# Performance work log

Measured on AMD Instinct MI355X. Metric: run time of the kernel, lower is better.

The kernel has to match this reference:

```python
import jax, jax.numpy as jnp
import numpy as np

CODEBOOK_SIZE = 1024
EMB_DIM = 64


def setup_inputs() -> dict:
    key = jax.random.key(0)
    k1, k2 = jax.random.split(key)
    z = jax.random.normal(k1, (4, EMB_DIM, 32, 32, 32), dtype=jnp.float32)
    embedding = jax.random.normal(k2, (CODEBOOK_SIZE, EMB_DIM), dtype=jnp.float32)
    return {"z": z, "embedding": embedding}


def reference(z, embedding):
    # z: [b, c, h, w, d], embedding: [K, c]
    b, c, h, w, d = z.shape
    K = embedding.shape[0]
    # flatten to [N, c] with channels last (matches permute(0,2,3,4,1).reshape)
    zf = jnp.transpose(z, (0, 2, 3, 4, 1)).reshape(-1, c)
    # squared L2 distance to each codebook entry: ||z||^2 - 2 z.e + ||e||^2
    dist = (
        jnp.sum(zf * zf, axis=1, keepdims=True)
        - 2.0 * zf @ embedding.T
        + jnp.sum(embedding * embedding, axis=1)[None, :]
    )  # [N, K]
    min_encoding_indices = jnp.argmin(dist, axis=1)  # [N]
    # one-hot @ embedding == gather (same math, no NxK materialization)
    z_q = embedding[min_encoding_indices]  # [N, c]
    z_q = jnp.transpose(z_q.reshape(b, h, w, d, c), (0, 4, 1, 2, 3))
    # straight-through estimator
    z_q = z + jax.lax.stop_gradient(z_q - z)
    # perplexity from mean one-hot occupancy
    n_tokens = zf.shape[0]
    e_mean = jnp.bincount(min_encoding_indices, length=K).astype(zf.dtype) / n_tokens
    perplexity = jnp.exp(-jnp.sum(e_mean * jnp.log(e_mean + 1e-10)))
    loss = jnp.asarray(0.0, dtype=z.dtype)
    return (
        z_q,
        loss,
        perplexity,
        min_encoding_indices.reshape(b, h, w, d),
        jnp.mean(dist),
    )
```

## Files before the change

kernel.cpp:

```cpp
#include <hip/hip_runtime.h>

#define CH     64
#define KC     1024
#define SP     32768
#define NBATCH 4
#define NTOK   (NBATCH * SP)
#define MTOK   64
#define SZZ    68
#define ECH    256
#define SZEB   72
#define CAP    16
#define MARGIN 3.0f

#define OFF_ZQ   0
#define OFF_LOSS (NBATCH * CH * SP)
#define OFF_PERP (OFF_LOSS + 1)
#define OFF_IDX  (OFF_PERP + 1)
#define OFF_MEAN (OFF_IDX + NTOK)


typedef __attribute__((ext_vector_type(8))) short  s16x8;
typedef __attribute__((ext_vector_type(4))) float  f32x4;

__device__ __forceinline__ unsigned short f2bf(float f) {
    unsigned int u = __float_as_uint(f);
    return (unsigned short)((u + 0x7fffu + ((u >> 16) & 1u)) >> 16);
}

__device__ __forceinline__ float exact_dist(const float* zrow,
                                            const float* __restrict__ emb,
                                            const float* enl, int c) {
    const float4* er = (const float4*)(emb + (size_t)c * CH);
    float a0 = 0.f, a1 = 0.f, a2 = 0.f, a3 = 0.f;
#pragma unroll
    for (int j = 0; j < 16; ++j) {
        float4 e4 = er[j];
        a0 = fmaf(zrow[4 * j + 0], e4.x, a0);
        a1 = fmaf(zrow[4 * j + 1], e4.y, a1);
        a2 = fmaf(zrow[4 * j + 2], e4.z, a2);
        a3 = fmaf(zrow[4 * j + 3], e4.w, a3);
    }
    return enl[c] - 2.f * ((a0 + a1) + (a2 + a3));
}

__global__ __launch_bounds__(256) void prep(const float* __restrict__ e,
                                            int* __restrict__ hist,
                                            float* __restrict__ sums,
                                            float* __restrict__ sum_zc,
                                            float* __restrict__ sum_ec,
                                            float* __restrict__ enorm,
                                            unsigned short* __restrict__ eb) {
    const int tid = threadIdx.x;
    const int bk = blockIdx.x;
    if (bk < 4) {
        int k = bk * 256 + tid;
        const float4* row = (const float4*)(e + (size_t)k * CH);
        float n = 0.f;
#pragma unroll
        for (int j = 0; j < CH / 4; ++j) {
            float4 v = row[j];
            n += v.x * v.x + v.y * v.y + v.z * v.z + v.w * v.w;
        }
        enorm[k] = n;
    } else if (bk == 4) {
        if (tid == 0) sums[0] = 0.f;
        if (tid < 64) sum_zc[tid] = 0.f;
        __shared__ float ls1[256];
        __shared__ float r2[4];
        int c = tid & 63;
        int strip = tid >> 6;
        float s1 = 0.f, s2 = 0.f;
        for (int k = strip * 256; k < strip * 256 + 256; ++k) {
            float v = e[k * CH + c];
            s1 += v;
            s2 = fmaf(v, v, s2);
        }
        ls1[tid] = s1;
        for (int off = 32; off; off >>= 1) s2 += __shfl_down(s2, off);
        if ((tid & 63) == 0) r2[tid >> 6] = s2;
        __syncthreads();
        if (strip == 0) sum_ec[c] = ls1[c] + ls1[64 + c] + ls1[128 + c] + ls1[192 + c];
        if (tid == 0) sums[1] = r2[0] + r2[1] + r2[2] + r2[3];
    } else if (bk < 9) {
        hist[(bk - 5) * 256 + tid] = 0;
    } else {
        int base = (bk - 9) * 16384;
        for (int j = 0; j < 64; ++j) {
            int i = base + tid + j * 256;
            eb[i] = f2bf(e[i]);
        }
    }
}

__global__ __launch_bounds__(256, 2) void vq_main(const float* __restrict__ z,
                                                  const float* __restrict__ emb,
                                                  const unsigned short* __restrict__ eb,
                                                  const float* __restrict__ enorm,
                                                  float* __restrict__ out,
                                                  int* __restrict__ hist,
                                                  float* __restrict__ sums,
                                                  float* __restrict__ sum_zc) {
    __shared__ float zl[MTOK * SZZ];
    __shared__ unsigned short ebl[ECH * SZEB];
    __shared__ float enorm_l[KC];
    __shared__ float dmin_l[MTOK];
    __shared__ float zs1[256], zs2[256];
    __shared__ int   cand[MTOK][CAP];
    __shared__ int   ccnt[MTOK];
    __shared__ int   fi[MTOK];

    const int tid = threadIdx.x;
    const int w = tid >> 6;
    const int lane = tid & 63;
    const int n15 = lane & 15;
    const int q = lane >> 4;
    const int t0 = blockIdx.x * MTOK;
    const int bb = t0 >> 15;
    const int s0 = t0 & (SP - 1);

    {
        const float* zbase = z + ((size_t)bb * CH) * SP + s0;
#pragma unroll
        for (int j = 0; j < 4; ++j) {
            int idx = tid + j * 256;
            int c = idx >> 4;
            int tq = idx & 15;
            float4 v = *(const float4*)(zbase + (size_t)c * SP + tq * 4);
            zl[(4 * tq + 0) * SZZ + c] = v.x;
            zl[(4 * tq + 1) * SZZ + c] = v.y;
            zl[(4 * tq + 2) * SZZ + c] = v.z;
            zl[(4 * tq + 3) * SZZ + c] = v.w;
        }
#pragma unroll
        for (int j = 0; j < 4; ++j) enorm_l[tid + j * 256] = enorm[tid + j * 256];
        if (tid < MTOK) ccnt[tid] = 0;
    }
    __syncthreads();

    s16x8 A0, A1;
    {
        const float* zrow = &zl[(w * 16 + n15) * SZZ];
        float4 za = *(const float4*)(zrow + q * 8);
        float4 zb = *(const float4*)(zrow + q * 8 + 4);
        float4 zc = *(const float4*)(zrow + 32 + q * 8);
        float4 zd = *(const float4*)(zrow + 32 + q * 8 + 4);
        A0[0] = (short)f2bf(za.x); A0[1] = (short)f2bf(za.y);
        A0[2] = (short)f2bf(za.z); A0[3] = (short)f2bf(za.w);
        A0[4] = (short)f2bf(zb.x); A0[5] = (short)f2bf(zb.y);
        A0[6] = (short)f2bf(zb.z); A0[7] = (short)f2bf(zb.w);
        A1[0] = (short)f2bf(zc.x); A1[1] = (short)f2bf(zc.y);
        A1[2] = (short)f2bf(zc.z); A1[3] = (short)f2bf(zc.w);
        A1[4] = (short)f2bf(zd.x); A1[5] = (short)f2bf(zd.y);
        A1[6] = (short)f2bf(zd.z); A1[7] = (short)f2bf(zd.w);
    }
    const unsigned short* ebq = ebl + (size_t)n15 * SZEB + q * 8;

    float bmin[4] = {3.4e38f, 3.4e38f, 3.4e38f, 3.4e38f};
    for (int ch = 0; ch < 4; ++ch) {
        __syncthreads();
#pragma unroll
        for (int rep = 0; rep < 8; ++rep) {
            int i = tid + rep * 256;
            int row = i >> 3, j = i & 7;
            ((float4*)&ebl[row * SZEB])[j] =
                ((const float4*)(eb + (size_t)(ch * ECH + row) * CH))[j];
        }
        __syncthreads();
        for (int ct = 0; ct < 16; ++ct) {
            const unsigned short* p = ebq + ct * 16 * SZEB;
            s16x8 B0 = *(const s16x8*)p;
            s16x8 B1 = *(const s16x8*)(p + 32);
            f32x4 acc = {0.f, 0.f, 0.f, 0.f};
            acc = __builtin_amdgcn_mfma_f32_16x16x32_bf16(A0, B0, acc, 0, 0, 0);
            acc = __builtin_amdgcn_mfma_f32_16x16x32_bf16(A1, B1, acc, 0, 0, 0);
            float en = enorm_l[ch * ECH + ct * 16 + n15];
#pragma unroll
            for (int r = 0; r < 4; ++r) {
                float d = fmaf(-2.f, acc[r], en);
                bmin[r] = fminf(bmin[r], d);
            }
        }
    }
#pragma unroll
    for (int off = 1; off < 16; off <<= 1)
#pragma unroll
        for (int r = 0; r < 4; ++r)
            bmin[r] = fminf(bmin[r], __shfl_xor(bmin[r], off));
    if (n15 == 0)
#pragma unroll
        for (int r = 0; r < 4; ++r) dmin_l[w * 16 + 4 * q + r] = bmin[r];
    __syncthreads();

    float thr[4];
#pragma unroll
    for (int r = 0; r < 4; ++r) thr[r] = dmin_l[w * 16 + 4 * q + r] + MARGIN;
    for (int cc = 0; cc < 4; ++cc) {
        int ch = (cc == 0) ? 3 : (cc - 1);
        if (cc) {
            __syncthreads();
#pragma unroll
            for (int rep = 0; rep < 8; ++rep) {
                int i = tid + rep * 256;
                int row = i >> 3, j = i & 7;
                ((float4*)&ebl[row * SZEB])[j] =
                    ((const float4*)(eb + (size_t)(ch * ECH + row) * CH))[j];
            }
            __syncthreads();
        }
        for (int ct = 0; ct < 16; ++ct) {
            const unsigned short* p = ebq + ct * 16 * SZEB;
            s16x8 B0 = *(const s16x8*)p;
            s16x8 B1 = *(const s16x8*)(p + 32);
            f32x4 acc = {0.f, 0.f, 0.f, 0.f};
            acc = __builtin_amdgcn_mfma_f32_16x16x32_bf16(A0, B0, acc, 0, 0, 0);
            acc = __builtin_amdgcn_mfma_f32_16x16x32_bf16(A1, B1, acc, 0, 0, 0);
            float en = enorm_l[ch * ECH + ct * 16 + n15];
#pragma unroll
            for (int r = 0; r < 4; ++r) {
                float d = fmaf(-2.f, acc[r], en);
                if (d <= thr[r]) {
                    int t = w * 16 + 4 * q + r;
                    int pos = atomicAdd(&ccnt[t], 1);
                    if (pos < CAP) cand[t][pos] = ch * ECH + ct * 16 + n15;
                }
            }
        }
    }
    __syncthreads();

    if (tid < MTOK) {
        int t = tid;
        const float* zrow = &zl[t * SZZ];
        int cnt = ccnt[t];
        float best = 3.4e38f;
        int bi = 0;
        if (cnt <= CAP) {
            for (int j = 0; j < cnt; ++j) {
                int c = cand[t][j];
                float d = exact_dist(zrow, emb, enorm_l, c);
                if (d < best || (d == best && c < bi)) { best = d; bi = c; }
            }
        } else {
            for (int c = 0; c < KC; ++c) {
                float d = exact_dist(zrow, emb, enorm_l, c);
                if (d < best) { best = d; bi = c; }
            }
        }
        fi[t] = bi;
        out[OFF_IDX + t0 + t] = (float)bi;
        atomicAdd(&hist[bi], 1);
    }
    __syncthreads();

#pragma unroll
    for (int j = 0; j < 16; ++j) {
        int idx = tid + j * 256;
        int c = idx >> 6;
        int t = idx & 63;
        int code = fi[t];
        float ev = emb[(size_t)code * CH + c];
        float zv = zl[t * SZZ + c];
        out[OFF_ZQ + ((size_t)bb * CH + c) * SP + s0 + t] = zv + (ev - zv);
    }

    {
        int c = tid >> 2, qq = tid & 3;
        float s1 = 0.f, s2 = 0.f;
        for (int tt = 0; tt < 16; ++tt) {
            float v = zl[(qq * 16 + tt) * SZZ + c];
            s1 += v;
            s2 = fmaf(v, v, s2);
        }
        zs1[tid] = s1;
        zs2[tid] = s2;
    }
    __syncthreads();
    if (tid < 64) {
        float a = zs1[4 * tid] + zs1[4 * tid + 1] + zs1[4 * tid + 2] + zs1[4 * tid + 3];
        atomicAdd(&sum_zc[tid], a);
        float bsum = zs2[4 * tid] + zs2[4 * tid + 1] + zs2[4 * tid + 2] + zs2[4 * tid + 3];
        for (int off = 32; off; off >>= 1) bsum += __shfl_down(bsum, off);
        if (tid == 0) atomicAdd(&sums[0], bsum);
    }
}

__global__ __launch_bounds__(1024) void finalize(const int* __restrict__ hist,
                                                 const float* __restrict__ sums,
                                                 const float* __restrict__ sum_zc,
                                                 const float* __restrict__ sum_ec,
                                                 float* __restrict__ out) {
    __shared__ float red[1024];
    int k = threadIdx.x;
    float p = (float)hist[k] * (1.0f / (float)NTOK);
    red[k] = p * logf(p + 1e-10f);
    __syncthreads();
    for (int off = 512; off; off >>= 1) {
        if (k < off) red[k] += red[k + off];
        __syncthreads();
    }
    if (k == 0) {
        out[OFF_PERP] = expf(-red[0]);
        out[OFF_LOSS] = 0.f;
        double dot = 0.0;
        for (int c = 0; c < CH; ++c) dot += (double)sum_zc[c] * (double)sum_ec[c];
        double mean = ((double)KC * (double)sums[0] + (double)NTOK * (double)sums[1] - 2.0 * dot)
                      / ((double)NTOK * (double)KC);
        out[OFF_MEAN] = (float)mean;
    }
}

extern "C" void kernel_launch(void* const* d_in, const int* in_sizes, int n_in,
                              void* d_out, int out_size, void* d_ws, size_t ws_size,
                              hipStream_t stream) {
    const float* z   = (const float*)d_in[0];
    const float* emb = (const float*)d_in[1];
    float* out = (float*)d_out;

    int*            hist   = (int*)d_ws;
    float*          sums   = (float*)d_ws + 1024;
    float*          sum_zc = (float*)d_ws + 1026;
    float*          sum_ec = (float*)d_ws + 1090;
    float*          enorm  = (float*)d_ws + 1154;
    unsigned short* eb     = (unsigned short*)((int*)d_ws + 4096);

    prep<<<13, 256, 0, stream>>>(emb, hist, sums, sum_zc, sum_ec, enorm, eb);
    vq_main<<<NTOK / MTOK, 256, 0, stream>>>(z, emb, eb, enorm, out, hist, sums, sum_zc);
    finalize<<<1, 1024, 0, stream>>>(hist, sums, sum_zc, sum_ec, out);
}
```

Before: 227.3 us.

## Double tokens per block and stream bf16 codebook from global memory without LDS staging

Each wave now handles 32 tokens instead of 16, so every codebook fragment feeds two MFMA pairs. The bf16 codebook and its norms are read straight from global/L2 rather than staged through shared memory, which removes the chunk loads and barriers from both MFMA passes. Dropping those LDS buffers lets occupancy rise to 4 blocks per CU. In exchange the kernel depends on the cache for codebook reuse, candidate capacity halves to 8 (so more tokens may hit the full 1024-code exact fallback), and the z-statistics scratch now reuses the candidate buffer.

```diff
diff --git a/kernel.cpp b/kernel.cpp
--- a/kernel.cpp
+++ b/kernel.cpp
@@ -5,11 +5,9 @@
 #define SP     32768
 #define NBATCH 4
 #define NTOK   (NBATCH * SP)
-#define MTOK   64
+#define MTOK   128
 #define SZZ    68
-#define ECH    256
-#define SZEB   72
-#define CAP    16
+#define CAP    8
 #define MARGIN 3.0f
 
 #define OFF_ZQ   0
@@ -29,7 +27,7 @@
 
 __device__ __forceinline__ float exact_dist(const float* zrow,
                                             const float* __restrict__ emb,
-                                            const float* enl, int c) {
+                                            const float* __restrict__ enl, int c) {
     const float4* er = (const float4*)(emb + (size_t)c * CH);
     float a0 = 0.f, a1 = 0.f, a2 = 0.f, a3 = 0.f;
 #pragma unroll
@@ -92,7 +90,17 @@
     }
 }
 
-__global__ __launch_bounds__(256, 2) void vq_main(const float* __restrict__ z,
+#define MK8(A, ptr)                                            \
+    {                                                          \
+        float4 _a = *(const float4*)(ptr);                     \
+        float4 _b = *(const float4*)((ptr) + 4);               \
+        A[0] = (short)f2bf(_a.x); A[1] = (short)f2bf(_a.y);    \
+        A[2] = (short)f2bf(_a.z); A[3] = (short)f2bf(_a.w);    \
+        A[4] = (short)f2bf(_b.x); A[5] = (short)f2bf(_b.y);    \
+        A[6] = (short)f2bf(_b.z); A[7] = (short)f2bf(_b.w);    \
+    }
+
+__global__ __launch_bounds__(256, 4) void vq_main(const float* __restrict__ z,
                                                   const float* __restrict__ emb,
                                                   const unsigned short* __restrict__ eb,
                                                   const float* __restrict__ enorm,
@@ -101,10 +109,6 @@
                                                   float* __restrict__ sums,
                                                   float* __restrict__ sum_zc) {
     __shared__ float zl[MTOK * SZZ];
-    __shared__ unsigned short ebl[ECH * SZEB];
-    __shared__ float enorm_l[KC];
-    __shared__ float dmin_l[MTOK];
-    __shared__ float zs1[256], zs2[256];
     __shared__ int   cand[MTOK][CAP];
     __shared__ int   ccnt[MTOK];
     __shared__ int   fi[MTOK];
@@ -121,108 +125,93 @@
     {
         const float* zbase = z + ((size_t)bb * CH) * SP + s0;
 #pragma unroll
-        for (int j = 0; j < 4; ++j) {
-            int idx = tid + j * 256;
-            int c = idx >> 4;
-            int tq = idx & 15;
+        for (int rep = 0; rep < 8; ++rep) {
+            int idx = tid + rep * 256;
+            int c = idx >> 5;
+            int tq = idx & 31;
             float4 v = *(const float4*)(zbase + (size_t)c * SP + tq * 4);
             zl[(4 * tq + 0) * SZZ + c] = v.x;
             zl[(4 * tq + 1) * SZZ + c] = v.y;
             zl[(4 * tq + 2) * SZZ + c] = v.z;
             zl[(4 * tq + 3) * SZZ + c] = v.w;
         }
-#pragma unroll
-        for (int j = 0; j < 4; ++j) enorm_l[tid + j * 256] = enorm[tid + j * 256];
         if (tid < MTOK) ccnt[tid] = 0;
     }
     __syncthreads();
 
-    s16x8 A0, A1;
+    s16x8 A0, A1, A2, A3;
     {
-        const float* zrow = &zl[(w * 16 + n15) * SZZ];
-        float4 za = *(const float4*)(zrow + q * 8);
-        float4 zb = *(const float4*)(zrow + q * 8 + 4);
-        float4 zc = *(const float4*)(zrow + 32 + q * 8);
-        float4 zd = *(const float4*)(zrow + 32 + q * 8 + 4);
-        A0[0] = (short)f2bf(za.x); A0[1] = (short)f2bf(za.y);
-        A0[2] = (short)f2bf(za.z); A0[3] = (short)f2bf(za.w);
-        A0[4] = (short)f2bf(zb.x); A0[5] = (short)f2bf(zb.y);
-        A0[6] = (short)f2bf(zb.z); A0[7] = (short)f2bf(zb.w);
-        A1[0] = (short)f2bf(zc.x); A1[1] = (short)f2bf(zc.y);
-        A1[2] = (short)f2bf(zc.z); A1[3] = (short)f2bf(zc.w);
-        A1[4] = (short)f2bf(zd.x); A1[5] = (short)f2bf(zd.y);
-        A1[6] = (short)f2bf(zd.z); A1[7] = (short)f2bf(zd.w);
-    }
-    const unsigned short* ebq = ebl + (size_t)n15 * SZEB + q * 8;
-
-    float bmin[4] = {3.4e38f, 3.4e38f, 3.4e38f, 3.4e38f};
-    for (int ch = 0; ch < 4; ++ch) {
-        __syncthreads();
-#pragma unroll
-        for (int rep = 0; rep < 8; ++rep) {
-            int i = tid + rep * 256;
-            int row = i >> 3, j = i & 7;
-            ((float4*)&ebl[row * SZEB])[j] =
-                ((const float4*)(eb + (size_t)(ch * ECH + row) * CH))[j];
-        }
-        __syncthreads();
-        for (int ct = 0; ct < 16; ++ct) {
-            const unsigned short* p = ebq + ct * 16 * SZEB;
-            s16x8 B0 = *(const s16x8*)p;
-            s16x8 B1 = *(const s16x8*)(p + 32);
-            f32x4 acc = {0.f, 0.f, 0.f, 0.f};
-            acc = __builtin_amdgcn_mfma_f32_16x16x32_bf16(A0, B0, acc, 0, 0, 0);
-            acc = __builtin_amdgcn_mfma_f32_16x16x32_bf16(A1, B1, acc, 0, 0, 0);
-            float en = enorm_l[ch * ECH + ct * 16 + n15];
-#pragma unroll
-            for (int r = 0; r < 4; ++r) {
-                float d = fmaf(-2.f, acc[r], en);
-                bmin[r] = fminf(bmin[r], d);
+        const float* zr0 = &zl[(w * 32 + n15) * SZZ];
+        const float* zr1 = zr0 + 16 * SZZ;
+        MK8(A0, zr0 + q * 8)
+        MK8(A1, zr0 + 32 + q * 8)
+        MK8(A2, zr1 + q * 8)
+        MK8(A3, zr1 + 32 + q * 8)
+    }
+
+    const unsigned short* ebp = eb + (size_t)n15 * CH + q * 8;
+    const float* enp = enorm + n15;
+
+    float bmin0[4] = {3.4e38f, 3.4e38f, 3.4e38f, 3.4e38f};
+    float bmin1[4] = {3.4e38f, 3.4e38f, 3.4e38f, 3.4e38f};
+#pragma unroll 4
+    for (int ct = 0; ct < 64; ++ct) {
+        const unsigned short* pr = ebp + (size_t)ct * (16 * CH);
+        s16x8 B0 = *(const s16x8*)pr;
+        s16x8 B1 = *(const s16x8*)(pr + 32);
+        float en = enp[ct * 16];
+        f32x4 acc0 = {0.f, 0.f, 0.f, 0.f};
+        f32x4 acc1 = {0.f, 0.f, 0.f, 0.f};
+        acc0 = __builtin_amdgcn_mfma_f32_16x16x32_bf16(A0, B0, acc0, 0, 0, 0);
+        acc0 = __builtin_amdgcn_mfma_f32_16x16x32_bf16(A1, B1, acc0, 0, 0, 0);
+        acc1 = __builtin_amdgcn_mfma_f32_16x16x32_bf16(A2, B0, acc1, 0, 0, 0);
+        acc1 = __builtin_amdgcn_mfma_f32_16x16x32_bf16(A3, B1, acc1, 0, 0, 0);
+#pragma unroll
+        for (int r = 0; r < 4; ++r) {
+            bmin0[r] = fminf(bmin0[r], fmaf(-2.f, acc0[r], en));
+            bmin1[r] = fminf(bmin1[r], fmaf(-2.f, acc1[r], en));
+        }
+    }
+#pragma unroll
+    for (int off = 1; off < 16; off <<= 1)
+#pragma unroll
+        for (int r = 0; r < 4; ++r) {
+            bmin0[r] = fminf(bmin0[r], __shfl_xor(bmin0[r], off));
+            bmin1[r] = fminf(bmin1[r], __shfl_xor(bmin1[r], off));
+        }
+    float thr0[4], thr1[4];
+#pragma unroll
+    for (int r = 0; r < 4; ++r) {
+        thr0[r] = bmin0[r] + MARGIN;
+        thr1[r] = bmin1[r] + MARGIN;
+    }
+
+    const int tb0 = w * 32 + 4 * q;
+    const int tb1 = tb0 + 16;
+#pragma unroll 4
+    for (int ct = 0; ct < 64; ++ct) {
+        const unsigned short* pr = ebp + (size_t)ct * (16 * CH);
+        s16x8 B0 = *(const s16x8*)pr;
+        s16x8 B1 = *(const s16x8*)(pr + 32);
+        float en = enp[ct * 16];
+        f32x4 acc0 = {0.f, 0.f, 0.f, 0.f};
+        f32x4 acc1 = {0.f, 0.f, 0.f, 0.f};
+        acc0 = __builtin_amdgcn_mfma_f32_16x16x32_bf16(A0, B0, acc0, 0, 0, 0);
+        acc0 = __builtin_amdgcn_mfma_f32_16x16x32_bf16(A1, B1, acc0, 0, 0, 0);
+        acc1 = __builtin_amdgcn_mfma_f32_16x16x32_bf16(A2, B0, acc1, 0, 0, 0);
+        acc1 = __builtin_amdgcn_mfma_f32_16x16x32_bf16(A3, B1, acc1, 0, 0, 0);
+        int code = ct * 16 + n15;
+#pragma unroll
+        for (int r = 0; r < 4; ++r) {
+            float d0 = fmaf(-2.f, acc0[r], en);
+            if (d0 <= thr0[r]) {
+                int pos = atomicAdd(&ccnt[tb0 + r], 1);
+                if (pos < CAP) cand[tb0 + r][pos] = code;
             }
-        }
-    }
-#pragma unroll
-    for (int off = 1; off < 16; off <<= 1)
-#pragma unroll
-        for (int r = 0; r < 4; ++r)
-            bmin[r] = fminf(bmin[r], __shfl_xor(bmin[r], off));
-    if (n15 == 0)
-#pragma unroll
-        for (int r = 0; r < 4; ++r) dmin_l[w * 16 + 4 * q + r] = bmin[r];
-    __syncthreads();
-
-    float thr[4];
-#pragma unroll
-    for (int r = 0; r < 4; ++r) thr[r] = dmin_l[w * 16 + 4 * q + r] + MARGIN;
-    for (int cc = 0; cc < 4; ++cc) {
-        int ch = (cc == 0) ? 3 : (cc - 1);
-        if (cc) {
-            __syncthreads();
-#pragma unroll
-            for (int rep = 0; rep < 8; ++rep) {
-                int i = tid + rep * 256;
-                int row = i >> 3, j = i & 7;
-                ((float4*)&ebl[row * SZEB])[j] =
-                    ((const float4*)(eb + (size_t)(ch * ECH + row) * CH))[j];
-            }
-            __syncthreads();
-        }
-        for (int ct = 0; ct < 16; ++ct) {
-            const unsigned short* p = ebq + ct * 16 * SZEB;
-            s16x8 B0 = *(const s16x8*)p;
-            s16x8 B1 = *(const s16x8*)(p + 32);
-            f32x4 acc = {0.f, 0.f, 0.f, 0.f};
-            acc = __builtin_amdgcn_mfma_f32_16x16x32_bf16(A0, B0, acc, 0, 0, 0);
-            acc = __builtin_amdgcn_mfma_f32_16x16x32_bf16(A1, B1, acc, 0, 0, 0);
-            float en = enorm_l[ch * ECH + ct * 16 + n15];
-#pragma unroll
-            for (int r = 0; r < 4; ++r) {
-                float d = fmaf(-2.f, acc[r], en);
-                if (d <= thr[r]) {
-                    int t = w * 16 + 4 * q + r;
-                    int pos = atomicAdd(&ccnt[t], 1);
-                    if (pos < CAP) cand[t][pos] = ch * ECH + ct * 16 + n15;
-                }
+            float d1 = fmaf(-2.f, acc1[r], en);
+            if (d1 <= thr1[r]) {
+                int pos = atomicAdd(&ccnt[tb1 + r], 1);
+                if (pos < CAP) cand[tb1 + r][pos] = code;
             }
         }
     }
@@ -237,12 +226,12 @@
         if (cnt <= CAP) {
             for (int j = 0; j < cnt; ++j) {
                 int c = cand[t][j];
-                float d = exact_dist(zrow, emb, enorm_l, c);
+                float d = exact_dist(zrow, emb, enorm, c);
                 if (d < best || (d == best && c < bi)) { best = d; bi = c; }
             }
         } else {
             for (int c = 0; c < KC; ++c) {
-                float d = exact_dist(zrow, emb, enorm_l, c);
+                float d = exact_dist(zrow, emb, enorm, c);
                 if (d < best) { best = d; bi = c; }
             }
         }
@@ -253,34 +242,39 @@
     __syncthreads();
 
 #pragma unroll
-    for (int j = 0; j < 16; ++j) {
-        int idx = tid + j * 256;
-        int c = idx >> 6;
-        int t = idx & 63;
+    for (int rep = 0; rep < 32; ++rep) {
+        int idx = tid + rep * 256;
+        int c = idx >> 7;
+        int t = idx & 127;
         int code = fi[t];
         float ev = emb[(size_t)code * CH + c];
         float zv = zl[t * SZZ + c];
         out[OFF_ZQ + ((size_t)bb * CH + c) * SP + s0 + t] = zv + (ev - zv);
     }
 
-    {
-        int c = tid >> 2, qq = tid & 3;
+    float* zs = reinterpret_cast<float*>(cand);
+#pragma unroll
+    for (int h = 0; h < 2; ++h) {
+        const int c = tid >> 2, qq = tid & 3;
         float s1 = 0.f, s2 = 0.f;
+#pragma unroll
         for (int tt = 0; tt < 16; ++tt) {
-            float v = zl[(qq * 16 + tt) * SZZ + c];
+            float v = zl[(h * 64 + qq * 16 + tt) * SZZ + c];
             s1 += v;
             s2 = fmaf(v, v, s2);
         }
-        zs1[tid] = s1;
-        zs2[tid] = s2;
-    }
-    __syncthreads();
-    if (tid < 64) {
-        float a = zs1[4 * tid] + zs1[4 * tid + 1] + zs1[4 * tid + 2] + zs1[4 * tid + 3];
-        atomicAdd(&sum_zc[tid], a);
-        float bsum = zs2[4 * tid] + zs2[4 * tid + 1] + zs2[4 * tid + 2] + zs2[4 * tid + 3];
-        for (int off = 32; off; off >>= 1) bsum += __shfl_down(bsum, off);
-        if (tid == 0) atomicAdd(&sums[0], bsum);
+        zs[tid] = s1;
+        zs[256 + tid] = s2;
+        __syncthreads();
+        if (tid < 64) {
+            float a = zs[4 * tid] + zs[4 * tid + 1] + zs[4 * tid + 2] + zs[4 * tid + 3];
+            atomicAdd(&sum_zc[tid], a);
+            float bsum = zs[256 + 4 * tid] + zs[256 + 4 * tid + 1]
+                       + zs[256 + 4 * tid + 2] + zs[256 + 4 * tid + 3];
+            for (int off = 32; off; off >>= 1) bsum += __shfl_down(bsum, off);
+            if (tid == 0) atomicAdd(&sums[0], bsum);
+        }
+        __syncthreads();
     }
 }
 
```

After: 609.1 us. 168% more time.

## Prefetch codebook chunks through registers with swizzled LDS and higher occupancy

Applied to the files above, without the earlier changes.

Halves the codebook chunk staged in LDS to 128 entries. While the MFMA work runs on the current chunk, the next chunk is loaded into registers and then written to LDS, so global loads overlap compute in both the min pass and the candidate pass. Row padding is replaced by an XOR swizzle to avoid bank conflicts. CAP is cut to 8 and the reduction scratch reuses the candidate buffer, so the smaller LDS footprint lets launch bounds ask for 4 blocks per CU. The trade-offs are more barriers per chunk, added register pressure from the prefetch, and a greater chance of falling back to the full exact scan when a token has more than 8 near candidates.

```diff
diff --git a/kernel.cpp b/kernel.cpp
--- a/kernel.cpp
+++ b/kernel.cpp
@@ -7,9 +7,8 @@
 #define NTOK   (NBATCH * SP)
 #define MTOK   64
 #define SZZ    68
-#define ECH    256
-#define SZEB   72
-#define CAP    16
+#define ECH    128
+#define CAP    8
 #define MARGIN 3.0f
 
 #define OFF_ZQ   0
@@ -92,7 +91,7 @@
     }
 }
 
-__global__ __launch_bounds__(256, 2) void vq_main(const float* __restrict__ z,
+__global__ __launch_bounds__(256, 4) void vq_main(const float* __restrict__ z,
                                                   const float* __restrict__ emb,
                                                   const unsigned short* __restrict__ eb,
                                                   const float* __restrict__ enorm,
@@ -101,10 +100,9 @@
                                                   float* __restrict__ sums,
                                                   float* __restrict__ sum_zc) {
     __shared__ float zl[MTOK * SZZ];
-    __shared__ unsigned short ebl[ECH * SZEB];
+    __shared__ __align__(16) unsigned short ebl[ECH * 64];
     __shared__ float enorm_l[KC];
     __shared__ float dmin_l[MTOK];
-    __shared__ float zs1[256], zs2[256];
     __shared__ int   cand[MTOK][CAP];
     __shared__ int   ccnt[MTOK];
     __shared__ int   fi[MTOK];
@@ -117,6 +115,25 @@
     const int t0 = blockIdx.x * MTOK;
     const int bb = t0 >> 15;
     const int s0 = t0 & (SP - 1);
+
+    const int sg  = tid & 7;
+    const int sr0 = tid >> 3;
+    const int sgd = sg ^ (sr0 & 7);
+    float4 g0, g1, g2, g3;
+#define STAGE_LOAD(cb)                                                      \
+    {                                                                       \
+        g0 = ((const float4*)(eb + (size_t)((cb) + sr0) * CH))[sg];         \
+        g1 = ((const float4*)(eb + (size_t)((cb) + sr0 + 32) * CH))[sg];    \
+        g2 = ((const float4*)(eb + (size_t)((cb) + sr0 + 64) * CH))[sg];    \
+        g3 = ((const float4*)(eb + (size_t)((cb) + sr0 + 96) * CH))[sg];    \
+    }
+#define STAGE_WRITE()                                                       \
+    {                                                                       \
+        ((float4*)&ebl[(size_t)sr0 * 64])[sgd] = g0;                        \
+        ((float4*)&ebl[(size_t)(sr0 + 32) * 64])[sgd] = g1;                 \
+        ((float4*)&ebl[(size_t)(sr0 + 64) * 64])[sgd] = g2;                 \
+        ((float4*)&ebl[(size_t)(sr0 + 96) * 64])[sgd] = g3;                 \
+    }
 
     {
         const float* zbase = z + ((size_t)bb * CH) * SP + s0;
@@ -134,6 +151,8 @@
 #pragma unroll
         for (int j = 0; j < 4; ++j) enorm_l[tid + j * 256] = enorm[tid + j * 256];
         if (tid < MTOK) ccnt[tid] = 0;
+        STAGE_LOAD(0)
+        STAGE_WRITE()
     }
     __syncthreads();
 
@@ -153,80 +172,76 @@
         A1[4] = (short)f2bf(zd.x); A1[5] = (short)f2bf(zd.y);
         A1[6] = (short)f2bf(zd.z); A1[7] = (short)f2bf(zd.w);
     }
-    const unsigned short* ebq = ebl + (size_t)n15 * SZEB + q * 8;
+    const int gsw = q ^ (n15 & 7);
 
     float bmin[4] = {3.4e38f, 3.4e38f, 3.4e38f, 3.4e38f};
-    for (int ch = 0; ch < 4; ++ch) {
-        __syncthreads();
-#pragma unroll
-        for (int rep = 0; rep < 8; ++rep) {
-            int i = tid + rep * 256;
-            int row = i >> 3, j = i & 7;
-            ((float4*)&ebl[row * SZEB])[j] =
-                ((const float4*)(eb + (size_t)(ch * ECH + row) * CH))[j];
-        }
-        __syncthreads();
-        for (int ct = 0; ct < 16; ++ct) {
-            const unsigned short* p = ebq + ct * 16 * SZEB;
-            s16x8 B0 = *(const s16x8*)p;
-            s16x8 B1 = *(const s16x8*)(p + 32);
+    for (int p = 0; p < 8; ++p) {
+        if (p < 7) STAGE_LOAD((p + 1) * ECH)
+        const int cb = p * ECH;
+#pragma unroll
+        for (int ct = 0; ct < 8; ++ct) {
+            const s16x8* rowp = (const s16x8*)&ebl[(size_t)(ct * 16 + n15) * 64];
+            s16x8 B0 = rowp[gsw];
+            s16x8 B1 = rowp[gsw ^ 4];
             f32x4 acc = {0.f, 0.f, 0.f, 0.f};
             acc = __builtin_amdgcn_mfma_f32_16x16x32_bf16(A0, B0, acc, 0, 0, 0);
             acc = __builtin_amdgcn_mfma_f32_16x16x32_bf16(A1, B1, acc, 0, 0, 0);
-            float en = enorm_l[ch * ECH + ct * 16 + n15];
+            float en = enorm_l[cb + ct * 16 + n15];
 #pragma unroll
             for (int r = 0; r < 4; ++r) {
                 float d = fmaf(-2.f, acc[r], en);
                 bmin[r] = fminf(bmin[r], d);
             }
         }
-    }
-#pragma unroll
-    for (int off = 1; off < 16; off <<= 1)
-#pragma unroll
-        for (int r = 0; r < 4; ++r)
-            bmin[r] = fminf(bmin[r], __shfl_xor(bmin[r], off));
-    if (n15 == 0)
-#pragma unroll
-        for (int r = 0; r < 4; ++r) dmin_l[w * 16 + 4 * q + r] = bmin[r];
-    __syncthreads();
+        if (p == 7) {
+#pragma unroll
+            for (int off = 1; off < 16; off <<= 1)
+#pragma unroll
+                for (int r = 0; r < 4; ++r)
+                    bmin[r] = fminf(bmin[r], __shfl_xor(bmin[r], off));
+            if (n15 == 0)
+#pragma unroll
+                for (int r = 0; r < 4; ++r) dmin_l[w * 16 + 4 * q + r] = bmin[r];
+        }
+        __syncthreads();
+        if (p < 7) {
+            STAGE_WRITE()
+            __syncthreads();
+        }
+    }
 
     float thr[4];
 #pragma unroll
     for (int r = 0; r < 4; ++r) thr[r] = dmin_l[w * 16 + 4 * q + r] + MARGIN;
-    for (int cc = 0; cc < 4; ++cc) {
-        int ch = (cc == 0) ? 3 : (cc - 1);
-        if (cc) {
-            __syncthreads();
-#pragma unroll
-            for (int rep = 0; rep < 8; ++rep) {
-                int i = tid + rep * 256;
-                int row = i >> 3, j = i & 7;
-                ((float4*)&ebl[row * SZEB])[j] =
-                    ((const float4*)(eb + (size_t)(ch * ECH + row) * CH))[j];
-            }
-            __syncthreads();
-        }
-        for (int ct = 0; ct < 16; ++ct) {
-            const unsigned short* p = ebq + ct * 16 * SZEB;
-            s16x8 B0 = *(const s16x8*)p;
-            s16x8 B1 = *(const s16x8*)(p + 32);
+    for (int p = 0; p < 8; ++p) {
+        const int chunk = (p == 0) ? 7 : (p - 1);
+        if (p < 7) STAGE_LOAD(p * ECH)
+        const int cb = chunk * ECH;
+#pragma unroll
+        for (int ct = 0; ct < 8; ++ct) {
+            const s16x8* rowp = (const s16x8*)&ebl[(size_t)(ct * 16 + n15) * 64];
+            s16x8 B0 = rowp[gsw];
+            s16x8 B1 = rowp[gsw ^ 4];
             f32x4 acc = {0.f, 0.f, 0.f, 0.f};
             acc = __builtin_amdgcn_mfma_f32_16x16x32_bf16(A0, B0, acc, 0, 0, 0);
             acc = __builtin_amdgcn_mfma_f32_16x16x32_bf16(A1, B1, acc, 0, 0, 0);
-            float en = enorm_l[ch * ECH + ct * 16 + n15];
+            float en = enorm_l[cb + ct * 16 + n15];
 #pragma unroll
             for (int r = 0; r < 4; ++r) {
                 float d = fmaf(-2.f, acc[r], en);
                 if (d <= thr[r]) {
                     int t = w * 16 + 4 * q + r;
                     int pos = atomicAdd(&ccnt[t], 1);
-                    if (pos < CAP) cand[t][pos] = ch * ECH + ct * 16 + n15;
+                    if (pos < CAP) cand[t][pos] = cb + ct * 16 + n15;
                 }
             }
         }
-    }
-    __syncthreads();
+        __syncthreads();
+        if (p < 7) {
+            STAGE_WRITE()
+            __syncthreads();
+        }
+    }
 
     if (tid < MTOK) {
         int t = tid;
@@ -264,6 +279,8 @@
     }
 
     {
+        float* zs1 = reinterpret_cast<float*>(cand);
+        float* zs2 = zs1 + 256;
         int c = tid >> 2, qq = tid & 3;
         float s1 = 0.f, s2 = 0.f;
         for (int tt = 0; tt < 16; ++tt) {
@@ -273,15 +290,17 @@
         }
         zs1[tid] = s1;
         zs2[tid] = s2;
-    }
-    __syncthreads();
-    if (tid < 64) {
-        float a = zs1[4 * tid] + zs1[4 * tid + 1] + zs1[4 * tid + 2] + zs1[4 * tid + 3];
-        atomicAdd(&sum_zc[tid], a);
-        float bsum = zs2[4 * tid] + zs2[4 * tid + 1] + zs2[4 * tid + 2] + zs2[4 * tid + 3];
-        for (int off = 32; off; off >>= 1) bsum += __shfl_down(bsum, off);
-        if (tid == 0) atomicAdd(&sums[0], bsum);
-    }
+        __syncthreads();
+        if (tid < 64) {
+            float a = zs1[4 * tid] + zs1[4 * tid + 1] + zs1[4 * tid + 2] + zs1[4 * tid + 3];
+            atomicAdd(&sum_zc[tid], a);
+            float bsum = zs2[4 * tid] + zs2[4 * tid + 1] + zs2[4 * tid + 2] + zs2[4 * tid + 3];
+            for (int off = 32; off; off >>= 1) bsum += __shfl_down(bsum, off);
+            if (tid == 0) atomicAdd(&sums[0], bsum);
+        }
+    }
+#undef STAGE_LOAD
+#undef STAGE_WRITE
 }
 
 __global__ __launch_bounds__(1024) void finalize(const int* __restrict__ hist,
```

New measurement: 546.3 us. +140.4%, slower.

## Stage codebook tiles with direct global-to-LDS loads and XOR swizzle, shrink LDS

Applied to the files above, without the earlier changes.

Codebook bf16 tiles are now copied straight from global memory into shared memory with global_load_lds 16-byte transfers, instead of going through registers. Row padding is replaced by an XOR swizzle of the 16-byte chunks to avoid bank conflicts. Shared memory is cut by dropping the enorm copy (now read from global), aliasing the reduction scratch onto the candidate buffer, and halving the candidate capacity to 8. A smaller CAP raises the chance that a token overflows and falls back to the slow full exact scan over all 1024 codes.

```diff
diff --git a/kernel.cpp b/kernel.cpp
--- a/kernel.cpp
+++ b/kernel.cpp
@@ -8,8 +8,7 @@
 #define MTOK   64
 #define SZZ    68
 #define ECH    256
-#define SZEB   72
-#define CAP    16
+#define CAP    8
 #define MARGIN 3.0f
 
 #define OFF_ZQ   0
@@ -29,7 +28,7 @@
 
 __device__ __forceinline__ float exact_dist(const float* zrow,
                                             const float* __restrict__ emb,
-                                            const float* enl, int c) {
+                                            const float* __restrict__ enl, int c) {
     const float4* er = (const float4*)(emb + (size_t)c * CH);
     float a0 = 0.f, a1 = 0.f, a2 = 0.f, a3 = 0.f;
 #pragma unroll
@@ -92,6 +91,11 @@
     }
 }
 
+#define GLD16(gsrc, ldst)                                                        \
+    __builtin_amdgcn_global_load_lds(                                            \
+        (const __attribute__((address_space(1))) unsigned int*)(gsrc),           \
+        (__attribute__((address_space(3))) unsigned int*)(ldst), 16, 0, 0)
+
 __global__ __launch_bounds__(256, 2) void vq_main(const float* __restrict__ z,
                                                   const float* __restrict__ emb,
                                                   const unsigned short* __restrict__ eb,
@@ -101,10 +105,8 @@
                                                   float* __restrict__ sums,
                                                   float* __restrict__ sum_zc) {
     __shared__ float zl[MTOK * SZZ];
-    __shared__ unsigned short ebl[ECH * SZEB];
-    __shared__ float enorm_l[KC];
+    __shared__ __align__(16) unsigned short ebl[ECH * 64];
     __shared__ float dmin_l[MTOK];
-    __shared__ float zs1[256], zs2[256];
     __shared__ int   cand[MTOK][CAP];
     __shared__ int   ccnt[MTOK];
     __shared__ int   fi[MTOK];
@@ -117,6 +119,18 @@
     const int t0 = blockIdx.x * MTOK;
     const int bb = t0 >> 15;
     const int s0 = t0 & (SP - 1);
+
+    const int srow = (w << 6) + (lane >> 3);
+    const size_t gofs = (size_t)(((lane & 7) ^ (lane >> 3)) << 3);
+#define STAGE(cb)                                                             \
+    {                                                                         \
+        _Pragma("unroll")                                                     \
+        for (int it = 0; it < 8; ++it) {                                      \
+            const unsigned short* gs =                                        \
+                eb + (size_t)((cb) + srow + it * 8) * CH + gofs;              \
+            GLD16(gs, (char*)ebl + (w << 13) + (it << 10));                   \
+        }                                                                     \
+    }
 
     {
         const float* zbase = z + ((size_t)bb * CH) * SP + s0;
@@ -131,8 +145,6 @@
             zl[(4 * tq + 2) * SZZ + c] = v.z;
             zl[(4 * tq + 3) * SZZ + c] = v.w;
         }
-#pragma unroll
-        for (int j = 0; j < 4; ++j) enorm_l[tid + j * 256] = enorm[tid + j * 256];
         if (tid < MTOK) ccnt[tid] = 0;
     }
     __syncthreads();
@@ -153,27 +165,21 @@
         A1[4] = (short)f2bf(zd.x); A1[5] = (short)f2bf(zd.y);
         A1[6] = (short)f2bf(zd.z); A1[7] = (short)f2bf(zd.w);
     }
-    const unsigned short* ebq = ebl + (size_t)n15 * SZEB + q * 8;
+    const int gsw = q ^ (n15 & 7);
 
     float bmin[4] = {3.4e38f, 3.4e38f, 3.4e38f, 3.4e38f};
     for (int ch = 0; ch < 4; ++ch) {
         __syncthreads();
-#pragma unroll
-        for (int rep = 0; rep < 8; ++rep) {
-            int i = tid + rep * 256;
-            int row = i >> 3, j = i & 7;
-            ((float4*)&ebl[row * SZEB])[j] =
-                ((const float4*)(eb + (size_t)(ch * ECH + row) * CH))[j];
-        }
+        STAGE(ch * ECH)
         __syncthreads();
         for (int ct = 0; ct < 16; ++ct) {
-            const unsigned short* p = ebq + ct * 16 * SZEB;
-            s16x8 B0 = *(const s16x8*)p;
-            s16x8 B1 = *(const s16x8*)(p + 32);
+            const s16x8* rowp = (const s16x8*)&ebl[(size_t)(ct * 16 + n15) << 6];
+            s16x8 B0 = rowp[gsw];
+            s16x8 B1 = rowp[gsw ^ 4];
             f32x4 acc = {0.f, 0.f, 0.f, 0.f};
             acc = __builtin_amdgcn_mfma_f32_16x16x32_bf16(A0, B0, acc, 0, 0, 0);
             acc = __builtin_amdgcn_mfma_f32_16x16x32_bf16(A1, B1, acc, 0, 0, 0);
-            float en = enorm_l[ch * ECH + ct * 16 + n15];
+            float en = enorm[ch * ECH + ct * 16 + n15];
 #pragma unroll
             for (int r = 0; r < 4; ++r) {
                 float d = fmaf(-2.f, acc[r], en);
@@ -198,23 +204,17 @@
         int ch = (cc == 0) ? 3 : (cc - 1);
         if (cc) {
             __syncthreads();
-#pragma unroll
-            for (int rep = 0; rep < 8; ++rep) {
-                int i = tid + rep * 256;
-                int row = i >> 3, j = i & 7;
-                ((float4*)&ebl[row * SZEB])[j] =
-                    ((const float4*)(eb + (size_t)(ch * ECH + row) * CH))[j];
-            }
+            STAGE(ch * ECH)
             __syncthreads();
         }
         for (int ct = 0; ct < 16; ++ct) {
-            const unsigned short* p = ebq + ct * 16 * SZEB;
-            s16x8 B0 = *(const s16x8*)p;
-            s16x8 B1 = *(const s16x8*)(p + 32);
+            const s16x8* rowp = (const s16x8*)&ebl[(size_t)(ct * 16 + n15) << 6];
+            s16x8 B0 = rowp[gsw];
+            s16x8 B1 = rowp[gsw ^ 4];
             f32x4 acc = {0.f, 0.f, 0.f, 0.f};
             acc = __builtin_amdgcn_mfma_f32_16x16x32_bf16(A0, B0, acc, 0, 0, 0);
             acc = __builtin_amdgcn_mfma_f32_16x16x32_bf16(A1, B1, acc, 0, 0, 0);
-            float en = enorm_l[ch * ECH + ct * 16 + n15];
+            float en = enorm[ch * ECH + ct * 16 + n15];
 #pragma unroll
             for (int r = 0; r < 4; ++r) {
                 float d = fmaf(-2.f, acc[r], en);
@@ -237,12 +237,12 @@
         if (cnt <= CAP) {
             for (int j = 0; j < cnt; ++j) {
                 int c = cand[t][j];
-                float d = exact_dist(zrow, emb, enorm_l, c);
+                float d = exact_dist(zrow, emb, enorm, c);
                 if (d < best || (d == best && c < bi)) { best = d; bi = c; }
             }
         } else {
             for (int c = 0; c < KC; ++c) {
-                float d = exact_dist(zrow, emb, enorm_l, c);
+                float d = exact_dist(zrow, emb, enorm, c);
                 if (d < best) { best = d; bi = c; }
             }
         }
@@ -264,6 +264,8 @@
     }
 
     {
+        float* zs1 = reinterpret_cast<float*>(cand);
+        float* zs2 = zs1 + 256;
         int c = tid >> 2, qq = tid & 3;
         float s1 = 0.f, s2 = 0.f;
         for (int tt = 0; tt < 16; ++tt) {
@@ -273,15 +275,16 @@
         }
         zs1[tid] = s1;
         zs2[tid] = s2;
-    }
-    __syncthreads();
-    if (tid < 64) {
-        float a = zs1[4 * tid] + zs1[4 * tid + 1] + zs1[4 * tid + 2] + zs1[4 * tid + 3];
-        atomicAdd(&sum_zc[tid], a);
-        float bsum = zs2[4 * tid] + zs2[4 * tid + 1] + zs2[4 * tid + 2] + zs2[4 * tid + 3];
-        for (int off = 32; off; off >>= 1) bsum += __shfl_down(bsum, off);
-        if (tid == 0) atomicAdd(&sums[0], bsum);
-    }
+        __syncthreads();
+        if (tid < 64) {
+            float a = zs1[4 * tid] + zs1[4 * tid + 1] + zs1[4 * tid + 2] + zs1[4 * tid + 3];
+            atomicAdd(&sum_zc[tid], a);
+            float bsum = zs2[4 * tid] + zs2[4 * tid + 1] + zs2[4 * tid + 2] + zs2[4 * tid + 3];
+            for (int off = 32; off; off >>= 1) bsum += __shfl_down(bsum, off);
+            if (tid == 0) atomicAdd(&sums[0], bsum);
+        }
+    }
+#undef STAGE
 }
 
 __global__ __launch_bounds__(1024) void finalize(const int* __restrict__ hist,
```

Result: slower. 562.6 us (+147.5%).
